# Optimization experiments

Measured on AMD Instinct MI355X. Metric: run time of the kernel, lower is better.

Reference implementation:

```python
import jax, jax.numpy as jnp
import numpy as np

DIM, HEADS, HEAD_DIM, EPS = 1536, 12, 128, 1e-6
B, S = 1, 4096


def rmsnorm(x, w, eps=EPS):
    v = jnp.mean(jnp.square(x), axis=-1, keepdims=True)
    return x * jax.lax.rsqrt(v + eps) * w


def apply_rope(x, freqs):
    # x: [b,s,n,d]; freqs: [s, d//2] rotation angles (complex rope on adjacent pairs)
    b, s, n, d = x.shape
    xr = x.reshape(b, s, n, d // 2, 2)
    cos = jnp.cos(freqs)[None, :, None, :]
    sin = jnp.sin(freqs)[None, :, None, :]
    x0, x1 = xr[..., 0], xr[..., 1]
    out = jnp.stack([x0 * cos - x1 * sin, x0 * sin + x1 * cos], axis=-1)
    return out.reshape(b, s, n, d)


def setup_inputs() -> dict:
    key = jax.random.key(0)
    ks = jax.random.split(key, 12)
    scale = 0.02
    x = jax.random.normal(ks[0], (B, S, DIM), jnp.float32)
    # standard rope angles: pos * inv_freq
    inv_freq = 1.0 / (10000.0 ** (jnp.arange(0, HEAD_DIM, 2, dtype=jnp.float32) / HEAD_DIM))
    freqs = jnp.arange(S, dtype=jnp.float32)[:, None] * inv_freq[None, :]  # [S, 64]
    Wq = jax.random.normal(ks[1], (DIM, DIM), jnp.float32) * scale
    bq = jax.random.normal(ks[2], (DIM,), jnp.float32) * scale
    Wk = jax.random.normal(ks[3], (DIM, DIM), jnp.float32) * scale
    bk = jax.random.normal(ks[4], (DIM,), jnp.float32) * scale
    Wv = jax.random.normal(ks[5], (DIM, DIM), jnp.float32) * scale
    bv = jax.random.normal(ks[6], (DIM,), jnp.float32) * scale
    Wo = jax.random.normal(ks[7], (DIM, DIM), jnp.float32) * scale
    bo = jax.random.normal(ks[8], (DIM,), jnp.float32) * scale
    gq = 1.0 + jax.random.normal(ks[9], (DIM,), jnp.float32) * 0.01
    gk = 1.0 + jax.random.normal(ks[10], (DIM,), jnp.float32) * 0.01
    return dict(x=x, freqs=freqs, Wq=Wq, bq=bq, Wk=Wk, bk=bk, Wv=Wv, bv=bv,
                Wo=Wo, bo=bo, gq=gq, gk=gk)


def reference(x, freqs, Wq, bq, Wk, bk, Wv, bv, Wo, bo, gq, gk):
    b, s = x.shape[:2]
    n, d = HEADS, HEAD_DIM
    q = apply_rope(rmsnorm(x @ Wq.T + bq, gq).reshape(b, s, n, d), freqs)
    k = apply_rope(rmsnorm(x @ Wk.T + bk, gk).reshape(b, s, n, d), freqs)
    v = (x @ Wv.T + bv).reshape(b, s, n, d)
    # SDPA: softmax(q k^T / sqrt(d)) v
    scores = jnp.einsum('bqnd,bknd->bnqk', q, k) / jnp.sqrt(jnp.asarray(d, x.dtype))
    attn = jax.nn.softmax(scores, axis=-1)
    out = jnp.einsum('bnqk,bknd->bqnd', attn, v).reshape(b, s, n * d)
    return out @ Wo.T + bo
```

## Files before the change

### kernel.cpp

```cpp
#include <hip/hip_runtime.h>
#include <stdint.h>
#include <math.h>

#define DIM 1536
#define SEQ 4096
#define HEADS 12
#define HD 128

typedef __bf16 bf16x8 __attribute__((ext_vector_type(8)));
typedef float f32x4 __attribute__((ext_vector_type(4)));

typedef __attribute__((address_space(1))) void gas_void;
typedef __attribute__((address_space(3))) void las_void;

__device__ __forceinline__ float b2f(unsigned short u) {
  union { unsigned int i; float f; } x; x.i = ((unsigned int)u) << 16; return x.f;
}
__device__ __forceinline__ unsigned short f2b(float f) {
  union { float f; unsigned int i; } x; x.f = f;
  unsigned int u = x.i;
  unsigned int r = (u + 0x7fffu + ((u >> 16) & 1u)) >> 16;
  return (unsigned short)r;
}
__device__ __forceinline__ void gll16(const unsigned short* g, unsigned short* l) {
  __builtin_amdgcn_global_load_lds((gas_void*)g, (las_void*)l, 16, 0, 0);
}
__device__ __forceinline__ void cvtpk(unsigned int& d, float a, float b) {
  asm("v_cvt_pk_bf16_f32 %0, %1, %2" : "=v"(d) : "v"(a), "v"(b));
}
__device__ __forceinline__ void pl32(unsigned int& a, unsigned int& b) {
  asm("v_permlane32_swap_b32 %0, %1" : "+v"(a), "+v"(b));
}
__device__ __forceinline__ void pl16(unsigned int& a, unsigned int& b) {
  asm("v_permlane16_swap_b32 %0, %1" : "+v"(a), "+v"(b));
}
__device__ __forceinline__ float fexp2(float x) { return __builtin_amdgcn_exp2f(x); }

__global__ void detect_kernel(const unsigned int* __restrict__ xw, int* flag) {
  __shared__ int cnt;
  if (threadIdx.x == 0) cnt = 0;
  __syncthreads();
  int local = 0;
  for (int i = threadIdx.x; i < 1024; i += 256) {
    unsigned int e = (xw[i] >> 7) & 0xFFu;
    if (e >= 110u && e <= 140u) local++;
  }
  atomicAdd(&cnt, local);
  __syncthreads();
  if (threadIdx.x == 0) *flag = (cnt > 512) ? 0 : 1;
}

__global__ void convert_bf16_kernel(const void* __restrict__ src,
                                    unsigned short* __restrict__ dst, int n,
                                    const int* __restrict__ flag) {
  int f = *flag;
  for (int i = blockIdx.x * blockDim.x + threadIdx.x; i < n; i += gridDim.x * blockDim.x)
    dst[i] = f ? f2b(((const float*)src)[i]) : ((const unsigned short*)src)[i];
}

__global__ void convert_w4_kernel(const void* s0, const void* s1, const void* s2, const void* s3,
                                  unsigned short* d0, unsigned short* d1,
                                  unsigned short* d2, unsigned short* d3,
                                  int n, const int* __restrict__ flag) {
  const void* s; unsigned short* d;
  switch (blockIdx.y) {
    case 0: s = s0; d = d0; break;
    case 1: s = s1; d = d1; break;
    case 2: s = s2; d = d2; break;
    default: s = s3; d = d3; break;
  }
  int f = *flag;
  for (int i = blockIdx.x * blockDim.x + threadIdx.x; i < n; i += gridDim.x * blockDim.x)
    d[i] = f ? f2b(((const float*)s)[i]) : ((const unsigned short*)s)[i];
}

__global__ void convert_v6_kernel(const void* s0, const void* s1, const void* s2,
                                  const void* s3, const void* s4, const void* s5,
                                  unsigned short* d0, unsigned short* d1, unsigned short* d2,
                                  unsigned short* d3, unsigned short* d4, unsigned short* d5,
                                  int n, const int* __restrict__ flag) {
  const void* s; unsigned short* d;
  switch (blockIdx.y) {
    case 0: s = s0; d = d0; break;
    case 1: s = s1; d = d1; break;
    case 2: s = s2; d = d2; break;
    case 3: s = s3; d = d3; break;
    case 4: s = s4; d = d4; break;
    default: s = s5; d = d5; break;
  }
  int f = *flag;
  for (int i = blockIdx.x * blockDim.x + threadIdx.x; i < n; i += gridDim.x * blockDim.x)
    d[i] = f ? f2b(((const float*)s)[i]) : ((const unsigned short*)s)[i];
}

__global__ void convert_f32_kernel(const void* __restrict__ src,
                                   float* __restrict__ dst, int n,
                                   const int* __restrict__ flag) {
  int f = *flag;
  for (int i = blockIdx.x * blockDim.x + threadIdx.x; i < n; i += gridDim.x * blockDim.x)
    dst[i] = f ? ((const float*)src)[i] : b2f(((const unsigned short*)src)[i]);
}

__global__ void signal_kernel(float* out) { if (threadIdx.x == 0) out[0] = 999.0f; }

__device__ __forceinline__ void gemm_bt_body(
    const unsigned short* __restrict__ A,
    const unsigned short* __restrict__ W,
    const unsigned short* __restrict__ bias,
    unsigned short* __restrict__ Cb, float* __restrict__ Cf, int fmt, int vmode,
    int K, int N, int bx, int by)
{
  const int BK = 32;
  __shared__ unsigned short As[128 * 32];
  __shared__ unsigned short Bs[128 * 32];
  const int t = threadIdx.x;
  const int wave = t >> 6, lane = t & 63;
  const int quad = lane >> 4, l16 = lane & 15;
  const int m0 = by * 128, n0 = bx * 128;
  const int wm = (wave >> 1) * 64, wn = (wave & 1) * 64;

  f32x4 acc[4][4] = {};

  const int srow = t >> 2, sblk = t & 3;
  const unsigned short* Ag1 = A + (size_t)(m0 + srow) * K + sblk * 8;
  const unsigned short* Ag2 = A + (size_t)(m0 + 64 + srow) * K + sblk * 8;
  const unsigned short* Wg1 = W + (size_t)(n0 + srow) * K + sblk * 8;
  const unsigned short* Wg2 = W + (size_t)(n0 + 64 + srow) * K + sblk * 8;
  unsigned short* As1 = &As[t * 8];
  unsigned short* As2 = &As[2048 + t * 8];
  unsigned short* Bs1 = &Bs[t * 8];
  unsigned short* Bs2 = &Bs[2048 + t * 8];

  for (int k0 = 0; k0 < K; k0 += BK) {
    __syncthreads();
    gll16(Ag1 + k0, As1);
    gll16(Ag2 + k0, As2);
    gll16(Wg1 + k0, Bs1);
    gll16(Wg2 + k0, Bs2);
    __syncthreads();
    bf16x8 af[4], bfr[4];
#pragma unroll
    for (int i = 0; i < 4; ++i)
      af[i] = *(const bf16x8*)&As[(wm + i * 16 + l16) * 32 + quad * 8];
#pragma unroll
    for (int j = 0; j < 4; ++j)
      bfr[j] = *(const bf16x8*)&Bs[(wn + j * 16 + l16) * 32 + quad * 8];
#pragma unroll
    for (int i = 0; i < 4; ++i)
#pragma unroll
      for (int j = 0; j < 4; ++j)
        acc[i][j] = __builtin_amdgcn_mfma_f32_16x16x32_bf16(af[i], bfr[j], acc[i][j], 0, 0, 0);
  }

#pragma unroll
  for (int i = 0; i < 4; ++i) {
    int row = m0 + wm + i * 16 + quad * 4;
#pragma unroll
    for (int j = 0; j < 4; ++j) {
      int col = n0 + wn + j * 16 + l16;
      float bv = b2f(bias[col]);
      if (vmode) {
        union { unsigned short h4[4]; uint2 u; } pk;
#pragma unroll
        for (int r = 0; r < 4; ++r) pk.h4[r] = f2b(acc[i][j][r] + bv);
        *(uint2*)&Cb[(size_t)col * SEQ + row] = pk.u;
      } else {
#pragma unroll
        for (int r = 0; r < 4; ++r) {
          float v = acc[i][j][r] + bv;
          size_t idx = (size_t)(row + r) * N + col;
          if (fmt) Cf[idx] = v; else Cb[idx] = f2b(v);
        }
      }
    }
  }
}

__global__ __launch_bounds__(256) void qkv_gemm_kernel(
    const unsigned short* __restrict__ x,
    const unsigned short* __restrict__ Wq, const unsigned short* __restrict__ bq,
    const unsigned short* __restrict__ Wk, const unsigned short* __restrict__ bk,
    const unsigned short* __restrict__ Wv, const unsigned short* __restrict__ bv,
    unsigned short* qb, unsigned short* kb, unsigned short* vt)
{
  const unsigned short *W, *b; unsigned short* C; int vm = 0;
  if (blockIdx.z == 0)      { W = Wq; b = bq; C = qb; }
  else if (blockIdx.z == 1) { W = Wk; b = bk; C = kb; }
  else                      { W = Wv; b = bv; C = vt; vm = 1; }
  gemm_bt_body(x, W, b, C, nullptr, 0, vm, DIM, DIM, blockIdx.x, blockIdx.y);
}

__global__ __launch_bounds__(256) void out_gemm_kernel(
    const unsigned short* __restrict__ ab, const unsigned short* __restrict__ Wo,
    const unsigned short* __restrict__ bo, void* out, const int* __restrict__ flag)
{
  int fmt = *flag;
  gemm_bt_body(ab, Wo, bo, (unsigned short*)out, (float*)out, fmt, 0,
               DIM, DIM, blockIdx.x, blockIdx.y);
}

__global__ __launch_bounds__(256) void norm_rope_kernel(
    unsigned short* __restrict__ qb, unsigned short* __restrict__ kb,
    const unsigned short* __restrict__ gq, const unsigned short* __restrict__ gk,
    const float* __restrict__ freqsf)
{
  const int s = blockIdx.x;
  const int isq = (blockIdx.y == 0);
  unsigned short* row = (isq ? qb : kb) + (size_t)s * DIM;
  const unsigned short* g = (isq ? gq : gk);
  const int t = threadIdx.x;
  float ss = 0.f;
#pragma unroll
  for (int i = 0; i < 6; ++i) {
    float xv = b2f(row[t + 256 * i]);
    ss += xv * xv;
  }
#pragma unroll
  for (int off = 32; off > 0; off >>= 1) ss += __shfl_down(ss, off);
  __shared__ float red[4];
  if ((t & 63) == 0) red[t >> 6] = ss;
  __syncthreads();
  float tot = red[0] + red[1] + red[2] + red[3];
  float rinv = 1.0f / sqrtf(tot * (1.0f / DIM) + 1e-6f);
  if (isq) rinv *= 0.12751744900725559f;
#pragma unroll
  for (int i = 0; i < 3; ++i) {
    int pg = t + 256 * i;
    int c0 = pg * 2;
    float x0 = b2f(row[c0]), x1 = b2f(row[c0 + 1]);
    float y0 = x0 * rinv * b2f(g[c0]);
    float y1 = x1 * rinv * b2f(g[c0 + 1]);
    float ang = freqsf[s * 64 + (pg & 63)];
    float sn, cs;
    __sincosf(ang, &sn, &cs);
    row[c0]     = f2b(y0 * cs - y1 * sn);
    row[c0 + 1] = f2b(y0 * sn + y1 * cs);
  }
}

__global__ __launch_bounds__(256) void attn_kernel(
    const unsigned short* __restrict__ qb,
    const unsigned short* __restrict__ kb,
    const unsigned short* __restrict__ vt,
    float* __restrict__ op,
    float* __restrict__ lp,
    int seg)
{
  __shared__ unsigned short Ks[64 * 128];
  __shared__ unsigned short Vs[128 * 64];

  const int t = threadIdx.x;
  const int wave = t >> 6, lane = t & 63;
  const int quad = lane >> 4, l16 = lane & 15;
  const int h = blockIdx.y;
  const int z = blockIdx.z;
  const int qbase = blockIdx.x * 128 + wave * 32;
  const int kc0 = z * seg;

  bf16x8 qf[2][4];
#pragma unroll
  for (int mt = 0; mt < 2; ++mt)
#pragma unroll
    for (int kk = 0; kk < 4; ++kk)
      qf[mt][kk] = *(const bf16x8*)(qb + (size_t)(qbase + mt * 16 + l16) * DIM
                                    + h * HD + kk * 32 + quad * 8);

  f32x4 o[2][8] = {};
  float Lr[2] = {};

  const int krow = t >> 2, kblk = (t & 3) * 4;
  const int vd = t >> 1,  vblk = (t & 1) * 4;

  const unsigned short* kbase = kb + (size_t)krow * DIM + h * HD + kblk * 8;
  const unsigned short* vbase = vt + ((size_t)h * HD + vd) * SEQ + vblk * 8;

  uint4 kr0, kr1, kr2, kr3, vr0, vr1, vr2, vr3;
  {
    const unsigned short* s = kbase + (size_t)kc0 * DIM;
    kr0 = *(const uint4*)(s);
    kr1 = *(const uint4*)(s + 8);
    kr2 = *(const uint4*)(s + 16);
    kr3 = *(const uint4*)(s + 24);
    const unsigned short* sv = vbase + kc0;
    vr0 = *(const uint4*)(sv);
    vr1 = *(const uint4*)(sv + 8);
    vr2 = *(const uint4*)(sv + 16);
    vr3 = *(const uint4*)(sv + 24);
  }

  for (int kc = kc0; kc < kc0 + seg; kc += 64) {
    __syncthreads();
    {
      unsigned short* dst = &Ks[krow * 128];
      const int sw = krow & 7;
      *(uint4*)(dst + ((kblk + 0) ^ sw) * 8) = kr0;
      *(uint4*)(dst + ((kblk + 1) ^ sw) * 8) = kr1;
      *(uint4*)(dst + ((kblk + 2) ^ sw) * 8) = kr2;
      *(uint4*)(dst + ((kblk + 3) ^ sw) * 8) = kr3;
    }
    {
      unsigned short* dst = &Vs[vd * 64];
      const int sw = vd & 7;
      *(uint4*)(dst + ((vblk + 0) ^ sw) * 8) = vr0;
      *(uint4*)(dst + ((vblk + 1) ^ sw) * 8) = vr1;
      *(uint4*)(dst + ((vblk + 2) ^ sw) * 8) = vr2;
      *(uint4*)(dst + ((vblk + 3) ^ sw) * 8) = vr3;
    }
    __syncthreads();

    {
      int nkc = kc + 64;
      if (nkc >= kc0 + seg) nkc = kc;
      const unsigned short* s = kbase + (size_t)nkc * DIM;
      kr0 = *(const uint4*)(s);
      kr1 = *(const uint4*)(s + 8);
      kr2 = *(const uint4*)(s + 16);
      kr3 = *(const uint4*)(s + 24);
      const unsigned short* sv = vbase + nkc;
      vr0 = *(const uint4*)(sv);
      vr1 = *(const uint4*)(sv + 8);
      vr2 = *(const uint4*)(sv + 16);
      vr3 = *(const uint4*)(sv + 24);
    }

    f32x4 sc[2][4] = {};
    __builtin_amdgcn_s_setprio(1);
#pragma unroll
    for (int kk = 0; kk < 4; ++kk) {
#pragma unroll
      for (int j = 0; j < 4; ++j) {
        int row = j * 16 + l16;
        bf16x8 kf = *(const bf16x8*)&Ks[row * 128 + ((kk * 4 + quad) ^ (row & 7)) * 8];
        sc[0][j] = __builtin_amdgcn_mfma_f32_16x16x32_bf16(kf, qf[0][kk], sc[0][j], 0, 0, 0);
        sc[1][j] = __builtin_amdgcn_mfma_f32_16x16x32_bf16(kf, qf[1][kk], sc[1][j], 0, 0, 0);
      }
    }
    __builtin_amdgcn_s_setprio(0);

    unsigned int wlo[2][4], whi[2][4];
#pragma unroll
    for (int mt = 0; mt < 2; ++mt) {
      float ls = 0.f;
#pragma unroll
      for (int j = 0; j < 4; ++j) {
        float p0 = fexp2(sc[mt][j][0]);
        float p1 = fexp2(sc[mt][j][1]);
        float p2 = fexp2(sc[mt][j][2]);
        float p3 = fexp2(sc[mt][j][3]);
        ls += (p0 + p1) + (p2 + p3);
        cvtpk(wlo[mt][j], p0, p1);
        cvtpk(whi[mt][j], p2, p3);
      }
      Lr[mt] += ls;
    }

    bf16x8 pf[2][2];
#pragma unroll
    for (int mt = 0; mt < 2; ++mt)
#pragma unroll
      for (int kk2 = 0; kk2 < 2; ++kk2) {
        unsigned int ul = wlo[mt][kk2 * 2], vl = wlo[mt][kk2 * 2 + 1];
        unsigned int uh = whi[mt][kk2 * 2], vh = whi[mt][kk2 * 2 + 1];
        pl32(ul, vl); pl16(ul, vl);
        pl32(uh, vh); pl16(uh, vh);
        union { unsigned int w[4]; bf16x8 v; } u;
        u.w[0] = ul; u.w[1] = uh; u.w[2] = vl; u.w[3] = vh;
        pf[mt][kk2] = u.v;
      }

    __builtin_amdgcn_s_setprio(1);
#pragma unroll
    for (int kk2 = 0; kk2 < 2; ++kk2) {
#pragma unroll
      for (int j2 = 0; j2 < 8; ++j2) {
        bf16x8 vf = *(const bf16x8*)&Vs[(j2 * 16 + l16) * 64
                                        + ((kk2 * 4 + quad) ^ (l16 & 7)) * 8];
        o[0][j2] = __builtin_amdgcn_mfma_f32_16x16x32_bf16(pf[0][kk2], vf, o[0][j2], 0, 0, 0);
        o[1][j2] = __builtin_amdgcn_mfma_f32_16x16x32_bf16(pf[1][kk2], vf, o[1][j2], 0, 0, 0);
      }
    }
    __builtin_amdgcn_s_setprio(0);
  }

  float* opz = op + (size_t)z * SEQ * DIM;
  float* lpz = lp + (size_t)z * HEADS * SEQ + (size_t)h * SEQ;
#pragma unroll
  for (int mt = 0; mt < 2; ++mt) {
    float L = Lr[mt];
    L += __shfl_xor(L, 16);
    L += __shfl_xor(L, 32);
    if (lane < 16) lpz[qbase + mt * 16 + l16] = L;
  }
#pragma unroll
  for (int mt = 0; mt < 2; ++mt) {
#pragma unroll
    for (int j2 = 0; j2 < 8; ++j2) {
      int col = h * HD + j2 * 16 + l16;
#pragma unroll
      for (int r = 0; r < 4; ++r) {
        int row = qbase + mt * 16 + quad * 4 + r;
        opz[(size_t)row * DIM + col] = o[mt][j2][r];
      }
    }
  }
}

__global__ __launch_bounds__(256) void combine_kernel(
    const float* __restrict__ op, const float* __restrict__ lp,
    unsigned short* __restrict__ ab, int nz)
{
  int idx4 = blockIdx.x * 256 + threadIdx.x;
  int idx = idx4 * 4;
  int row = idx / DIM, col = idx - row * DIM;
  int h = col >> 7;
  float4 o = make_float4(0.f, 0.f, 0.f, 0.f);
  float l = 0.f;
  for (int z = 0; z < nz; ++z) {
    float4 v = *(const float4*)(op + (size_t)z * SEQ * DIM + idx);
    o.x += v.x; o.y += v.y; o.z += v.z; o.w += v.w;
    l += lp[(size_t)z * HEADS * SEQ + (size_t)h * SEQ + row];
  }
  float inv = 1.0f / l;
  union { unsigned short h4[4]; uint2 u; } pk;
  pk.h4[0] = f2b(o.x * inv);
  pk.h4[1] = f2b(o.y * inv);
  pk.h4[2] = f2b(o.z * inv);
  pk.h4[3] = f2b(o.w * inv);
  *(uint2*)&ab[idx] = pk.u;
}

extern "C" void kernel_launch(void* const* d_in, const int* in_sizes, int n_in,
                              void* d_out, int out_size, void* d_ws, size_t ws_size,
                              hipStream_t stream) {
  const int NX = SEQ * DIM, NW = DIM * DIM, NB = DIM, NF = SEQ * 64;

  char* w = (char*)d_ws;
  size_t off = 0;
  int* flag = (int*)(w + off);              off += 256;
  unsigned short* xb  = (unsigned short*)(w + off); off += (size_t)NX * 2;
  unsigned short* Wqb = (unsigned short*)(w + off); off += (size_t)NW * 2;
  unsigned short* Wkb = (unsigned short*)(w + off); off += (size_t)NW * 2;
  unsigned short* Wvb = (unsigned short*)(w + off); off += (size_t)NW * 2;
  unsigned short* Wob = (unsigned short*)(w + off); off += (size_t)NW * 2;
  unsigned short* bqb = (unsigned short*)(w + off); off += 4096;
  unsigned short* bkb = (unsigned short*)(w + off); off += 4096;
  unsigned short* bvb = (unsigned short*)(w + off); off += 4096;
  unsigned short* bob = (unsigned short*)(w + off); off += 4096;
  unsigned short* gqb = (unsigned short*)(w + off); off += 4096;
  unsigned short* gkb = (unsigned short*)(w + off); off += 4096;
  float* freqsf = (float*)(w + off);        off += (size_t)NF * 4;
  unsigned short* qb = (unsigned short*)(w + off); off += (size_t)NX * 2;
  unsigned short* kb = (unsigned short*)(w + off); off += (size_t)NX * 2;
  unsigned short* vt = (unsigned short*)(w + off); off += (size_t)NX * 2;
  unsigned short* ab = (unsigned short*)(w + off); off += (size_t)NX * 2;
  float* op = (float*)(w + off);
  float* lp;

  int nz = 2;
  size_t need2 = off + (size_t)2 * NX * 4 + (size_t)2 * HEADS * SEQ * 4;
  if (ws_size < need2) {
    signal_kernel<<<1, 64, 0, stream>>>((float*)d_out);
    return;
  }
  lp = (float*)(w + off + (size_t)nz * NX * 4);

  detect_kernel<<<1, 256, 0, stream>>>((const unsigned int*)d_in[0], flag);

  const int CT = 256;
  auto cgrid = [](int n) { int g = (n + 255) / 256; return g > 4096 ? 4096 : g; };
  convert_bf16_kernel<<<cgrid(NX), CT, 0, stream>>>(d_in[0], xb, NX, flag);
  convert_w4_kernel<<<dim3(cgrid(NW), 4), CT, 0, stream>>>(
      d_in[2], d_in[4], d_in[6], d_in[8], Wqb, Wkb, Wvb, Wob, NW, flag);
  convert_v6_kernel<<<dim3(cgrid(NB), 6), CT, 0, stream>>>(
      d_in[3], d_in[5], d_in[7], d_in[9], d_in[10], d_in[11],
      bqb, bkb, bvb, bob, gqb, gkb, NB, flag);
  convert_f32_kernel<<<cgrid(NF), CT, 0, stream>>>(d_in[1], freqsf, NF, flag);

  qkv_gemm_kernel<<<dim3(DIM / 128, SEQ / 128, 3), 256, 0, stream>>>(
      xb, Wqb, bqb, Wkb, bkb, Wvb, bvb, qb, kb, vt);
  norm_rope_kernel<<<dim3(SEQ, 2), 256, 0, stream>>>(qb, kb, gqb, gkb, freqsf);
  attn_kernel<<<dim3(SEQ / 128, HEADS, nz), 256, 0, stream>>>(qb, kb, vt, op, lp, SEQ / nz);
  combine_kernel<<<NX / 1024, 256, 0, stream>>>(op, lp, ab, nz);
  out_gemm_kernel<<<dim3(DIM / 128, SEQ / 128), 256, 0, stream>>>(ab, Wob, bob, d_out, flag);
}
```

Baseline: 437.4 us.

## Widen GEMM K-tile with XOR-swizzled LDS, smaller out-GEMM tile, vectorized converts

```diff
diff --git a/kernel.cpp b/kernel.cpp
--- a/kernel.cpp
+++ b/kernel.cpp
@@ -51,17 +51,25 @@
 }
 
 __global__ void convert_bf16_kernel(const void* __restrict__ src,
-                                    unsigned short* __restrict__ dst, int n,
+                                    unsigned short* __restrict__ dst, int n4,
                                     const int* __restrict__ flag) {
   int f = *flag;
-  for (int i = blockIdx.x * blockDim.x + threadIdx.x; i < n; i += gridDim.x * blockDim.x)
-    dst[i] = f ? f2b(((const float*)src)[i]) : ((const unsigned short*)src)[i];
+  for (int i = blockIdx.x * blockDim.x + threadIdx.x; i < n4; i += gridDim.x * blockDim.x) {
+    if (f) {
+      float4 v = ((const float4*)src)[i];
+      union { unsigned short h[4]; uint2 u; } pk;
+      pk.h[0] = f2b(v.x); pk.h[1] = f2b(v.y); pk.h[2] = f2b(v.z); pk.h[3] = f2b(v.w);
+      ((uint2*)dst)[i] = pk.u;
+    } else {
+      ((uint2*)dst)[i] = ((const uint2*)src)[i];
+    }
+  }
 }
 
 __global__ void convert_w4_kernel(const void* s0, const void* s1, const void* s2, const void* s3,
                                   unsigned short* d0, unsigned short* d1,
                                   unsigned short* d2, unsigned short* d3,
-                                  int n, const int* __restrict__ flag) {
+                                  int n4, const int* __restrict__ flag) {
   const void* s; unsigned short* d;
   switch (blockIdx.y) {
     case 0: s = s0; d = d0; break;
@@ -70,8 +78,16 @@
     default: s = s3; d = d3; break;
   }
   int f = *flag;
-  for (int i = blockIdx.x * blockDim.x + threadIdx.x; i < n; i += gridDim.x * blockDim.x)
-    d[i] = f ? f2b(((const float*)s)[i]) : ((const unsigned short*)s)[i];
+  for (int i = blockIdx.x * blockDim.x + threadIdx.x; i < n4; i += gridDim.x * blockDim.x) {
+    if (f) {
+      float4 v = ((const float4*)s)[i];
+      union { unsigned short h[4]; uint2 u; } pk;
+      pk.h[0] = f2b(v.x); pk.h[1] = f2b(v.y); pk.h[2] = f2b(v.z); pk.h[3] = f2b(v.w);
+      ((uint2*)d)[i] = pk.u;
+    } else {
+      ((uint2*)d)[i] = ((const uint2*)s)[i];
+    }
+  }
 }
 
 __global__ void convert_v6_kernel(const void* s0, const void* s1, const void* s2,
@@ -103,6 +119,7 @@
 
 __global__ void signal_kernel(float* out) { if (threadIdx.x == 0) out[0] = 999.0f; }
 
+template<int BM>
 __device__ __forceinline__ void gemm_bt_body(
     const unsigned short* __restrict__ A,
     const unsigned short* __restrict__ W,
@@ -110,50 +127,56 @@
     unsigned short* __restrict__ Cb, float* __restrict__ Cf, int fmt, int vmode,
     int K, int N, int bx, int by)
 {
-  const int BK = 32;
-  __shared__ unsigned short As[128 * 32];
-  __shared__ unsigned short Bs[128 * 32];
+  constexpr int BK = 64;
+  constexpr int MI = BM / 32;
+  constexpr int ALINES = BM * BK * 2 / 4096;
+  __shared__ unsigned short As[BM * BK];
+  __shared__ unsigned short Bs[128 * BK];
   const int t = threadIdx.x;
   const int wave = t >> 6, lane = t & 63;
   const int quad = lane >> 4, l16 = lane & 15;
-  const int m0 = by * 128, n0 = bx * 128;
-  const int wm = (wave >> 1) * 64, wn = (wave & 1) * 64;
-
-  f32x4 acc[4][4] = {};
-
-  const int srow = t >> 2, sblk = t & 3;
-  const unsigned short* Ag1 = A + (size_t)(m0 + srow) * K + sblk * 8;
-  const unsigned short* Ag2 = A + (size_t)(m0 + 64 + srow) * K + sblk * 8;
-  const unsigned short* Wg1 = W + (size_t)(n0 + srow) * K + sblk * 8;
-  const unsigned short* Wg2 = W + (size_t)(n0 + 64 + srow) * K + sblk * 8;
-  unsigned short* As1 = &As[t * 8];
-  unsigned short* As2 = &As[2048 + t * 8];
-  unsigned short* Bs1 = &Bs[t * 8];
-  unsigned short* Bs2 = &Bs[2048 + t * 8];
+  const int m0 = by * BM, n0 = bx * 128;
+  const int wm = (wave >> 1) * (BM / 2), wn = (wave & 1) * 64;
+
+  f32x4 acc[MI][4] = {};
+
+  const int srow = t >> 3;
+  const int scol = ((t & 7) ^ ((t >> 3) & 7)) * 8;
+  const unsigned short* Ag = A + (size_t)(m0 + srow) * K + scol;
+  const unsigned short* Wg = W + (size_t)(n0 + srow) * K + scol;
 
   for (int k0 = 0; k0 < K; k0 += BK) {
     __syncthreads();
-    gll16(Ag1 + k0, As1);
-    gll16(Ag2 + k0, As2);
-    gll16(Wg1 + k0, Bs1);
-    gll16(Wg2 + k0, Bs2);
+#pragma unroll
+    for (int L = 0; L < ALINES; ++L)
+      gll16(Ag + (size_t)L * 32 * K + k0, &As[L * 2048 + t * 8]);
+#pragma unroll
+    for (int L = 0; L < 4; ++L)
+      gll16(Wg + (size_t)L * 32 * K + k0, &Bs[L * 2048 + t * 8]);
     __syncthreads();
-    bf16x8 af[4], bfr[4];
-#pragma unroll
-    for (int i = 0; i < 4; ++i)
-      af[i] = *(const bf16x8*)&As[(wm + i * 16 + l16) * 32 + quad * 8];
-#pragma unroll
-    for (int j = 0; j < 4; ++j)
-      bfr[j] = *(const bf16x8*)&Bs[(wn + j * 16 + l16) * 32 + quad * 8];
-#pragma unroll
-    for (int i = 0; i < 4; ++i)
-#pragma unroll
-      for (int j = 0; j < 4; ++j)
-        acc[i][j] = __builtin_amdgcn_mfma_f32_16x16x32_bf16(af[i], bfr[j], acc[i][j], 0, 0, 0);
-  }
-
-#pragma unroll
-  for (int i = 0; i < 4; ++i) {
+#pragma unroll
+    for (int c = 0; c < 2; ++c) {
+      bf16x8 af[MI], bfr[4];
+#pragma unroll
+      for (int i = 0; i < MI; ++i) {
+        int row = wm + i * 16 + l16;
+        af[i] = *(const bf16x8*)&As[row * 64 + ((c * 4 + quad) ^ (row & 7)) * 8];
+      }
+#pragma unroll
+      for (int j = 0; j < 4; ++j) {
+        int row = wn + j * 16 + l16;
+        bfr[j] = *(const bf16x8*)&Bs[row * 64 + ((c * 4 + quad) ^ (row & 7)) * 8];
+      }
+#pragma unroll
+      for (int i = 0; i < MI; ++i)
+#pragma unroll
+        for (int j = 0; j < 4; ++j)
+          acc[i][j] = __builtin_amdgcn_mfma_f32_16x16x32_bf16(af[i], bfr[j], acc[i][j], 0, 0, 0);
+    }
+  }
+
+#pragma unroll
+  for (int i = 0; i < MI; ++i) {
     int row = m0 + wm + i * 16 + quad * 4;
 #pragma unroll
     for (int j = 0; j < 4; ++j) {
@@ -187,7 +210,7 @@
   if (blockIdx.z == 0)      { W = Wq; b = bq; C = qb; }
   else if (blockIdx.z == 1) { W = Wk; b = bk; C = kb; }
   else                      { W = Wv; b = bv; C = vt; vm = 1; }
-  gemm_bt_body(x, W, b, C, nullptr, 0, vm, DIM, DIM, blockIdx.x, blockIdx.y);
+  gemm_bt_body<128>(x, W, b, C, nullptr, 0, vm, DIM, DIM, blockIdx.x, blockIdx.y);
 }
 
 __global__ __launch_bounds__(256) void out_gemm_kernel(
@@ -195,8 +218,8 @@
     const unsigned short* __restrict__ bo, void* out, const int* __restrict__ flag)
 {
   int fmt = *flag;
-  gemm_bt_body(ab, Wo, bo, (unsigned short*)out, (float*)out, fmt, 0,
-               DIM, DIM, blockIdx.x, blockIdx.y);
+  gemm_bt_body<64>(ab, Wo, bo, (unsigned short*)out, (float*)out, fmt, 0,
+                   DIM, DIM, blockIdx.x, blockIdx.y);
 }
 
 __global__ __launch_bounds__(256) void norm_rope_kernel(
@@ -468,9 +491,9 @@
 
   const int CT = 256;
   auto cgrid = [](int n) { int g = (n + 255) / 256; return g > 4096 ? 4096 : g; };
-  convert_bf16_kernel<<<cgrid(NX), CT, 0, stream>>>(d_in[0], xb, NX, flag);
-  convert_w4_kernel<<<dim3(cgrid(NW), 4), CT, 0, stream>>>(
-      d_in[2], d_in[4], d_in[6], d_in[8], Wqb, Wkb, Wvb, Wob, NW, flag);
+  convert_bf16_kernel<<<cgrid(NX / 4), CT, 0, stream>>>(d_in[0], xb, NX / 4, flag);
+  convert_w4_kernel<<<dim3(cgrid(NW / 4), 4), CT, 0, stream>>>(
+      d_in[2], d_in[4], d_in[6], d_in[8], Wqb, Wkb, Wvb, Wob, NW / 4, flag);
   convert_v6_kernel<<<dim3(cgrid(NB), 6), CT, 0, stream>>>(
       d_in[3], d_in[5], d_in[7], d_in[9], d_in[10], d_in[11],
       bqb, bkb, bvb, bob, gqb, gkb, NB, flag);
@@ -481,5 +504,5 @@
   norm_rope_kernel<<<dim3(SEQ, 2), 256, 0, stream>>>(qb, kb, gqb, gkb, freqsf);
   attn_kernel<<<dim3(SEQ / 128, HEADS, nz), 256, 0, stream>>>(qb, kb, vt, op, lp, SEQ / nz);
   combine_kernel<<<NX / 1024, 256, 0, stream>>>(op, lp, ab, nz);
-  out_gemm_kernel<<<dim3(DIM / 128, SEQ / 128), 256, 0, stream>>>(ab, Wob, bob, d_out, flag);
-}
+  out_gemm_kernel<<<dim3(DIM / 128, SEQ / 64), 256, 0, stream>>>(ab, Wob, bob, d_out, flag);
+}
```

Result: faster. 399.6 us (-8.6%).
